# Kernel optimization log

Measured on AMD Instinct MI355X. Metric: run time of the kernel, lower is better.

Reference implementation:

```python
import jax, jax.numpy as jnp
import numpy as np

N_NODES = 50000
N_EDGES = 800000
IN_DIM = 256
HID = 128


def setup_inputs() -> dict:
    key = jax.random.key(0)
    ks = jax.random.split(key, 8)
    x = jax.random.normal(ks[0], (N_NODES, IN_DIM), dtype=jnp.float32)
    edge_index = jax.random.randint(ks[1], (2, N_EDGES), 0, N_NODES, dtype=jnp.int32)
    edge_weight = jax.random.uniform(ks[2], (N_EDGES,), dtype=jnp.float32)
    # xavier_normal with gain=1.414 as in torch init
    g = 1.414
    W1 = jax.random.normal(ks[3], (HID, IN_DIM), dtype=jnp.float32) * (g * np.sqrt(2.0 / (HID + IN_DIM)))
    W2 = jax.random.normal(ks[4], (HID, HID), dtype=jnp.float32) * (g * np.sqrt(2.0 / (HID + HID)))
    b1 = jnp.zeros((HID,), dtype=jnp.float32)
    b2 = jnp.zeros((HID,), dtype=jnp.float32)
    a1 = jnp.full((1,), 0.25, dtype=jnp.float32)  # nn.PReLU() default init
    a2 = jnp.full((1,), 0.25, dtype=jnp.float32)
    return {"x": x, "edge_index": edge_index, "edge_weight": edge_weight,
            "W1": W1, "b1": b1, "a1": a1, "W2": W2, "b2": b2, "a2": a2}


def _gcn_layer(z, W, b, a, src, dst, w):
    # linear (no bias): [N, out]
    fts = z @ W.T
    # spmm: out[dst] += w * fts[src]
    msg = fts[src] * w[:, None]                      # [E, out]
    out = jax.ops.segment_sum(msg, dst, num_segments=N_NODES) + b
    # PReLU (single shared parameter)
    return jnp.where(out >= 0, out, a * out)


def reference(x, edge_index, edge_weight, W1, b1, a1, W2, b2, a2):
    src, dst = edge_index[0], edge_index[1]
    z = _gcn_layer(x, W1, b1, a1, src, dst, edge_weight)
    z = _gcn_layer(z, W2, b2, a2, src, dst, edge_weight)
    return z
```

## Files before the change

### kernel.cpp

```cpp
#include <hip/hip_runtime.h>
#include <hip/hip_bf16.h>

#define HID 128
#define BSH 6
#define BSZ 64
#define NBMAX 1024
#define HB 64

typedef unsigned int uint;
typedef unsigned short ushort;
typedef __attribute__((ext_vector_type(8))) short short8;
typedef __attribute__((ext_vector_type(4))) float f32x4;

__device__ __forceinline__ ushort bf16_of(float x) {
    return __bfloat16_as_ushort(__float2bfloat16(x));
}

__device__ __forceinline__ uint pack_bf16x2(float a, float b) {
    return (uint)bf16_of(a) | ((uint)bf16_of(b) << 16);
}

union FragAB { uint4 u; short8 s; };

__global__ __launch_bounds__(256) void pack_hist(
    const float* __restrict__ W1, const float* __restrict__ W2,
    ushort* __restrict__ Wb1, ushort* __restrict__ Wb2,
    const int* __restrict__ dst, int* __restrict__ hpart, int E, int NB) {
    int blk = blockIdx.x;
    if (blk >= 24) {
        __shared__ int h[NBMAX];
        int hb = blk - 24;
        for (int i = threadIdx.x; i < NB; i += 256) h[i] = 0;
        __syncthreads();
        int chunk = (E + HB - 1) / HB;
        int c0 = hb * chunk;
        int c1 = min(c0 + chunk, E);
        for (int e = c0 + threadIdx.x; e < c1; e += 256)
            atomicAdd(&h[dst[e] >> BSH], 1);
        __syncthreads();
        for (int i = threadIdx.x; i < NB; i += 256) hpart[hb * NBMAX + i] = h[i];
        return;
    }
    const float* W = (blk < 16) ? W1 : W2;
    ushort* Wb = (blk < 16) ? Wb1 : Wb2;
    int K = (blk < 16) ? 256 : 128;
    int t = ((blk < 16) ? blk : blk - 16) * 256 + threadIdx.x;
    int lane = t & 63, f = t >> 6;
    int s = f >> 3, c = f & 7;
    int m = c * 16 + (lane & 15);
    int k0 = s * 32 + (lane >> 4) * 8;
    const float* wr = W + (size_t)m * K + k0;
    float4 a = *(const float4*)wr;
    float4 b = *(const float4*)(wr + 4);
    uint4 o = make_uint4(pack_bf16x2(a.x, a.y), pack_bf16x2(a.z, a.w),
                         pack_bf16x2(b.x, b.y), pack_bf16x2(b.z, b.w));
    *(uint4*)(Wb + (size_t)t * 8) = o;
}

template <int K, bool ABF16>
__device__ __forceinline__ FragAB load_afrag(const void* __restrict__ Xv, int row,
                                             int k0, bool ok) {
    FragAB af;
    if (ABF16) {
        af.u = ok ? *(const uint4*)((const ushort*)Xv + (size_t)row * K + k0)
                  : make_uint4(0, 0, 0, 0);
    } else {
        float4 va = make_float4(0.f, 0.f, 0.f, 0.f), vb = va;
        if (ok) {
            const float* xr = (const float*)Xv + (size_t)row * K + k0;
            va = *(const float4*)xr;
            vb = *(const float4*)(xr + 4);
        }
        af.u = make_uint4(pack_bf16x2(va.x, va.y), pack_bf16x2(va.z, va.w),
                          pack_bf16x2(vb.x, vb.y), pack_bf16x2(vb.z, vb.w));
    }
    return af;
}

template <int K, bool ABF16>
__global__ __launch_bounds__(256) void gemm_mfma(
    const void* __restrict__ Xv, const ushort* __restrict__ Wb,
    ushort* __restrict__ out, int N) {
    const int lane = threadIdx.x & 63;
    const int wid  = threadIdx.x >> 6;
    const int n0   = blockIdx.x * 128 + wid * 32;
    const int r0 = n0 + (lane & 15);
    const int r1 = r0 + 16;
    const bool ok0 = r0 < N, ok1 = r1 < N;
    const int kgrp = (lane >> 4) * 8;

    f32x4 acc0[8], acc1[8];
#pragma unroll
    for (int c = 0; c < 8; ++c) {
        acc0[c] = (f32x4){0.f, 0.f, 0.f, 0.f};
        acc1[c] = (f32x4){0.f, 0.f, 0.f, 0.f};
    }

#pragma unroll
    for (int s = 0; s < K / 32; ++s) {
        const int k0 = s * 32 + kgrp;
        FragAB a0 = load_afrag<K, ABF16>(Xv, r0, k0, ok0);
        FragAB a1 = load_afrag<K, ABF16>(Xv, r1, k0, ok1);
#pragma unroll
        for (int c = 0; c < 8; ++c) {
            FragAB bfr;
            bfr.u = *(const uint4*)(Wb + (size_t)((s * 8 + c) * 64 + lane) * 8);
            acc0[c] = __builtin_amdgcn_mfma_f32_16x16x32_bf16(a0.s, bfr.s, acc0[c], 0, 0, 0);
            acc1[c] = __builtin_amdgcn_mfma_f32_16x16x32_bf16(a1.s, bfr.s, acc1[c], 0, 0, 0);
        }
    }
    const int col = lane & 15;
    const int rb0 = n0 + (lane >> 4) * 4;
#pragma unroll
    for (int c = 0; c < 8; ++c) {
#pragma unroll
        for (int r = 0; r < 4; ++r) {
            int na = rb0 + r;
            if (na < N) out[(size_t)na * HID + c * 16 + col] = bf16_of(acc0[c][r]);
            int nb = na + 16;
            if (nb < N) out[(size_t)nb * HID + c * 16 + col] = bf16_of(acc1[c][r]);
        }
    }
}

__global__ __launch_bounds__(NBMAX) void bucket_scan(const int* __restrict__ hpart,
                                                     int* __restrict__ gbase,
                                                     int* __restrict__ gcur, int NB, int E) {
    __shared__ int l[NBMAX];
    int t = threadIdx.x;
    int v = 0;
    if (t < NB)
        for (int b = 0; b < HB; ++b) v += hpart[b * NBMAX + t];
    l[t] = v;
    __syncthreads();
    int x = v;
    for (int o = 1; o < NBMAX; o <<= 1) {
        int y = (t >= o) ? l[t - o] : 0;
        __syncthreads();
        x += y;
        l[t] = x;
        __syncthreads();
    }
    if (t < NB) { gbase[t] = x - v; gcur[t] = x - v; }
    if (t == 0) gbase[NB] = E;
}

__global__ __launch_bounds__(256) void bucket_stage(
    const int* __restrict__ src, const int* __restrict__ dst,
    const float* __restrict__ w, int* __restrict__ gcur,
    int2* __restrict__ staged, int E, int NB) {
    __shared__ int lh[NBMAX], lb[NBMAX];
    for (int i = threadIdx.x; i < NB; i += 256) lh[i] = 0;
    __syncthreads();
    int chunk = (E + gridDim.x - 1) / gridDim.x;
    int c0 = blockIdx.x * chunk;
    int c1 = min(c0 + chunk, E);
    for (int e = c0 + threadIdx.x; e < c1; e += 256)
        atomicAdd(&lh[dst[e] >> BSH], 1);
    __syncthreads();
    for (int i = threadIdx.x; i < NB; i += 256) {
        int c = lh[i];
        lb[i] = c ? atomicAdd(&gcur[i], c) : 0;
        lh[i] = 0;
    }
    __syncthreads();
    for (int e = c0 + threadIdx.x; e < c1; e += 256) {
        int d = dst[e];
        int b = d >> BSH;
        int slot = lb[b] + atomicAdd(&lh[b], 1);
        staged[slot] = make_int2(src[e] | ((d & (BSZ - 1)) << 16), __float_as_int(w[e]));
    }
}

__global__ __launch_bounds__(256) void node_sort(
    const int* __restrict__ gbase, const int2* __restrict__ staged,
    int2* __restrict__ csr, int* __restrict__ off, int N) {
    __shared__ int hist[BSZ];
    __shared__ int cur[BSZ];
    const int b = blockIdx.x;
    const int s0 = gbase[b], s1 = gbase[b + 1];
    const int t = threadIdx.x;
    if (t < BSZ) hist[t] = 0;
    __syncthreads();
    for (int e = s0 + t; e < s1; e += 256)
        atomicAdd(&hist[(staged[e].x >> 16) & (BSZ - 1)], 1);
    __syncthreads();
    if (t < BSZ) {
        int x = hist[t];
        int incl = x;
#pragma unroll
        for (int o = 1; o < BSZ; o <<= 1) {
            int y = __shfl_up(incl, o, BSZ);
            if (t >= o) incl += y;
        }
        int excl = incl - x;
        cur[t] = excl;
        int n = (b << BSH) + t;
        if (n <= N) off[n] = s0 + excl;
    }
    __syncthreads();
    for (int e = s0 + t; e < s1; e += 256) {
        int2 m = staged[e];
        int d = (m.x >> 16) & (BSZ - 1);
        int p = atomicAdd(&cur[d], 1);
        csr[s0 + p] = m;
    }
}

template <bool OUTBF16>
__global__ __launch_bounds__(256) void csr_gather_bf16(
    const int* __restrict__ off, const int2* __restrict__ edges,
    const ushort* __restrict__ fts, void* __restrict__ outv,
    const float* __restrict__ bias, const float* __restrict__ alpha, int N) {
    int d = blockIdx.x * 4 + (threadIdx.x >> 6);
    if (d >= N) return;
    const int lane = threadIdx.x & 63;
    const int g = lane >> 4;
    const int sub = lane & 15;
    int p = off[d];
    const int end = off[d + 1];
    float acc[8];
#pragma unroll
    for (int j = 0; j < 8; ++j) acc[j] = 0.f;

#define LOBITS(u_) __uint_as_float((u_) << 16)
#define HIBITS(u_) __uint_as_float((u_) & 0xffff0000u)
#define ROWOF(M_) (*(const uint4*)(fts + (size_t)((M_).x & 0xffff) * HID + sub * 8))
#define ACC8(R_, W_)                                              \
    do {                                                          \
        acc[0] += (W_) * LOBITS((R_).x); acc[1] += (W_) * HIBITS((R_).x); \
        acc[2] += (W_) * LOBITS((R_).y); acc[3] += (W_) * HIBITS((R_).y); \
        acc[4] += (W_) * LOBITS((R_).z); acc[5] += (W_) * HIBITS((R_).z); \
        acc[6] += (W_) * LOBITS((R_).w); acc[7] += (W_) * HIBITS((R_).w); \
    } while (0)

    for (; p + 16 <= end; p += 16) {
        int2 m0 = edges[p + g], m1 = edges[p + 4 + g];
        int2 m2 = edges[p + 8 + g], m3 = edges[p + 12 + g];
        uint4 r0 = ROWOF(m0), r1 = ROWOF(m1), r2 = ROWOF(m2), r3 = ROWOF(m3);
        float w0 = __int_as_float(m0.y), w1 = __int_as_float(m1.y);
        float w2 = __int_as_float(m2.y), w3 = __int_as_float(m3.y);
        ACC8(r0, w0); ACC8(r1, w1); ACC8(r2, w2); ACC8(r3, w3);
    }
    for (; p + 8 <= end; p += 8) {
        int2 ma = edges[p + g];
        int2 mb = edges[p + 4 + g];
        uint4 ra = ROWOF(ma), rb = ROWOF(mb);
        float wa = __int_as_float(ma.y), wb = __int_as_float(mb.y);
        ACC8(ra, wa);
        ACC8(rb, wb);
    }
    for (; p < end; p += 4) {
        int i = p + g;
        int2 m = edges[(i < end) ? i : (end - 1)];
        float wt = (i < end) ? __int_as_float(m.y) : 0.f;
        uint4 r = ROWOF(m);
        ACC8(r, wt);
    }
#undef ACC8
#undef ROWOF
#undef LOBITS
#undef HIBITS

#pragma unroll
    for (int j = 0; j < 8; ++j) {
        acc[j] += __shfl_xor(acc[j], 16);
        acc[j] += __shfl_xor(acc[j], 32);
    }

    const float a = alpha[0];
#pragma unroll
    for (int j = 0; j < 8; ++j) {
        float v = acc[j] + bias[sub * 8 + j];
        acc[j] = v >= 0.f ? v : a * v;
    }
    if (g == 0) {
        if (OUTBF16) {
            uint4 o = make_uint4(pack_bf16x2(acc[0], acc[1]), pack_bf16x2(acc[2], acc[3]),
                                 pack_bf16x2(acc[4], acc[5]), pack_bf16x2(acc[6], acc[7]));
            *(uint4*)((ushort*)outv + (size_t)d * HID + sub * 8) = o;
        } else {
            float* op = (float*)outv + (size_t)d * HID + sub * 8;
            *(float4*)op = make_float4(acc[0], acc[1], acc[2], acc[3]);
            *(float4*)(op + 4) = make_float4(acc[4], acc[5], acc[6], acc[7]);
        }
    }
}

extern "C" void kernel_launch(void* const* d_in, const int* in_sizes, int n_in,
                              void* d_out, int out_size, void* d_ws, size_t ws_size,
                              hipStream_t stream) {
    const float* x  = (const float*)d_in[0];
    const int*   ei = (const int*)d_in[1];
    const float* ew = (const float*)d_in[2];
    const float* W1 = (const float*)d_in[3];
    const float* b1 = (const float*)d_in[4];
    const float* a1 = (const float*)d_in[5];
    const float* W2 = (const float*)d_in[6];
    const float* b2 = (const float*)d_in[7];
    const float* a2 = (const float*)d_in[8];
    float* out = (float*)d_out;

    int N = in_sizes[0] / 256;
    int E = in_sizes[2];
    const int* src = ei;
    const int* dst = ei + E;
    int NB = (N + BSZ - 1) >> BSH;

    ushort* fts    = (ushort*)d_ws;
    ushort* agg    = fts + (size_t)N * HID;
    int2*   staged = (int2*)(agg + (size_t)N * HID);
    int2*   csr    = staged + E;
    ushort* Wb1    = (ushort*)(csr + E);
    ushort* Wb2    = Wb1 + 128 * 256;
    int*    hpart  = (int*)(Wb2 + 128 * 128);
    int*    gbase  = hpart + HB * NBMAX;
    int*    gcur   = gbase + NBMAX + 1;
    int*    off    = gcur + NBMAX;

    pack_hist<<<24 + HB, 256, 0, stream>>>(W1, W2, Wb1, Wb2, dst, hpart, E, NB);

    bucket_scan<<<1, NBMAX, 0, stream>>>(hpart, gbase, gcur, NB, E);
    bucket_stage<<<128, 256, 0, stream>>>(src, dst, ew, gcur, staged, E, NB);
    node_sort<<<NB, 256, 0, stream>>>(gbase, staged, csr, off, N);

    int gblk = (N + 127) / 128;
    int ggrid = (N + 3) / 4;

    gemm_mfma<256, false><<<gblk, 256, 0, stream>>>(x, Wb1, fts, N);
    csr_gather_bf16<true><<<ggrid, 256, 0, stream>>>(off, csr, fts, agg, b1, a1, N);

    gemm_mfma<128, true><<<gblk, 256, 0, stream>>>(agg, Wb2, fts, N);
    csr_gather_bf16<false><<<ggrid, 256, 0, stream>>>(off, csr, fts, out, b2, a2, N);
}
```

Before: 154.0 us.

## Fuse layer-1 GEMM with edge bucket staging into one heterogeneous launch

Merges the first-layer MFMA GEMM and the bucket_stage edge scatter into a single kernel whose blocks are split by block index, so the compute-bound GEMM and the atomic-heavy staging can run concurrently on the GPU. This removes one launch and the serialization between two independent stages. In exchange, the GEMM blocks now carry the staging kernel's 8KB static shared memory, which may reduce occupancy, and the GEMM blocks are scheduled before the staging blocks.

```diff
diff --git a/kernel.cpp b/kernel.cpp
--- a/kernel.cpp
+++ b/kernel.cpp
@@ -6,6 +6,7 @@
 #define BSZ 64
 #define NBMAX 1024
 #define HB 64
+#define STAGE_BLKS 128
 
 typedef unsigned int uint;
 typedef unsigned short ushort;
@@ -78,12 +79,12 @@
 }
 
 template <int K, bool ABF16>
-__global__ __launch_bounds__(256) void gemm_mfma(
+__device__ __forceinline__ void gemm_body(
     const void* __restrict__ Xv, const ushort* __restrict__ Wb,
-    ushort* __restrict__ out, int N) {
+    ushort* __restrict__ out, int N, int bid) {
     const int lane = threadIdx.x & 63;
     const int wid  = threadIdx.x >> 6;
-    const int n0   = blockIdx.x * 128 + wid * 32;
+    const int n0   = bid * 128 + wid * 32;
     const int r0 = n0 + (lane & 15);
     const int r1 = r0 + 16;
     const bool ok0 = r0 < N, ok1 = r1 < N;
@@ -121,6 +122,54 @@
             if (nb < N) out[(size_t)nb * HID + c * 16 + col] = bf16_of(acc1[c][r]);
         }
     }
+}
+
+__device__ __forceinline__ void stage_body(
+    const int* __restrict__ src, const int* __restrict__ dst,
+    const float* __restrict__ w, int* __restrict__ gcur,
+    int2* __restrict__ staged, int E, int NB, int bid) {
+    __shared__ int lh[NBMAX], lb[NBMAX];
+    for (int i = threadIdx.x; i < NB; i += 256) lh[i] = 0;
+    __syncthreads();
+    int chunk = (E + STAGE_BLKS - 1) / STAGE_BLKS;
+    int c0 = bid * chunk;
+    int c1 = min(c0 + chunk, E);
+    for (int e = c0 + threadIdx.x; e < c1; e += 256)
+        atomicAdd(&lh[dst[e] >> BSH], 1);
+    __syncthreads();
+    for (int i = threadIdx.x; i < NB; i += 256) {
+        int c = lh[i];
+        lb[i] = c ? atomicAdd(&gcur[i], c) : 0;
+        lh[i] = 0;
+    }
+    __syncthreads();
+    for (int e = c0 + threadIdx.x; e < c1; e += 256) {
+        int d = dst[e];
+        int b = d >> BSH;
+        int slot = lb[b] + atomicAdd(&lh[b], 1);
+        staged[slot] = make_int2(src[e] | ((d & (BSZ - 1)) << 16), __float_as_int(w[e]));
+    }
+}
+
+__global__ __launch_bounds__(256) void gemm1_stage(
+    const float* __restrict__ X, const ushort* __restrict__ Wb1,
+    ushort* __restrict__ fts, int N, int gblk,
+    const int* __restrict__ src, const int* __restrict__ dst,
+    const float* __restrict__ w, int* __restrict__ gcur,
+    int2* __restrict__ staged, int E, int NB) {
+    int bid = blockIdx.x;
+    if (bid < gblk) {
+        gemm_body<256, false>(X, Wb1, fts, N, bid);
+    } else {
+        stage_body(src, dst, w, gcur, staged, E, NB, bid - gblk);
+    }
+}
+
+template <int K, bool ABF16>
+__global__ __launch_bounds__(256) void gemm_mfma(
+    const void* __restrict__ Xv, const ushort* __restrict__ Wb,
+    ushort* __restrict__ out, int N) {
+    gemm_body<K, ABF16>(Xv, Wb, out, N, blockIdx.x);
 }
 
 __global__ __launch_bounds__(NBMAX) void bucket_scan(const int* __restrict__ hpart,
@@ -143,33 +192,6 @@
     }
     if (t < NB) { gbase[t] = x - v; gcur[t] = x - v; }
     if (t == 0) gbase[NB] = E;
-}
-
-__global__ __launch_bounds__(256) void bucket_stage(
-    const int* __restrict__ src, const int* __restrict__ dst,
-    const float* __restrict__ w, int* __restrict__ gcur,
-    int2* __restrict__ staged, int E, int NB) {
-    __shared__ int lh[NBMAX], lb[NBMAX];
-    for (int i = threadIdx.x; i < NB; i += 256) lh[i] = 0;
-    __syncthreads();
-    int chunk = (E + gridDim.x - 1) / gridDim.x;
-    int c0 = blockIdx.x * chunk;
-    int c1 = min(c0 + chunk, E);
-    for (int e = c0 + threadIdx.x; e < c1; e += 256)
-        atomicAdd(&lh[dst[e] >> BSH], 1);
-    __syncthreads();
-    for (int i = threadIdx.x; i < NB; i += 256) {
-        int c = lh[i];
-        lb[i] = c ? atomicAdd(&gcur[i], c) : 0;
-        lh[i] = 0;
-    }
-    __syncthreads();
-    for (int e = c0 + threadIdx.x; e < c1; e += 256) {
-        int d = dst[e];
-        int b = d >> BSH;
-        int slot = lb[b] + atomicAdd(&lh[b], 1);
-        staged[slot] = make_int2(src[e] | ((d & (BSZ - 1)) << 16), __float_as_int(w[e]));
-    }
 }
 
 __global__ __launch_bounds__(256) void node_sort(
@@ -318,18 +340,15 @@
     int*    gcur   = gbase + NBMAX + 1;
     int*    off    = gcur + NBMAX;
 
-    pack_hist<<<24 + HB, 256, 0, stream>>>(W1, W2, Wb1, Wb2, dst, hpart, E, NB);
-
-    bucket_scan<<<1, NBMAX, 0, stream>>>(hpart, gbase, gcur, NB, E);
-    bucket_stage<<<128, 256, 0, stream>>>(src, dst, ew, gcur, staged, E, NB);
-    node_sort<<<NB, 256, 0, stream>>>(gbase, staged, csr, off, N);
-
     int gblk = (N + 127) / 128;
     int ggrid = (N + 3) / 4;
 
-    gemm_mfma<256, false><<<gblk, 256, 0, stream>>>(x, Wb1, fts, N);
+    pack_hist<<<24 + HB, 256, 0, stream>>>(W1, W2, Wb1, Wb2, dst, hpart, E, NB);
+    bucket_scan<<<1, NBMAX, 0, stream>>>(hpart, gbase, gcur, NB, E);
+    gemm1_stage<<<gblk + STAGE_BLKS, 256, 0, stream>>>(
+        x, Wb1, fts, N, gblk, src, dst, ew, gcur, staged, E, NB);
+    node_sort<<<NB, 256, 0, stream>>>(gbase, staged, csr, off, N);
     csr_gather_bf16<true><<<ggrid, 256, 0, stream>>>(off, csr, fts, agg, b1, a1, N);
-
     gemm_mfma<128, true><<<gblk, 256, 0, stream>>>(agg, Wb2, fts, N);
     csr_gather_bf16<false><<<ggrid, 256, 0, stream>>>(off, csr, fts, out, b2, a2, N);
 }
```

Result: faster. 141.7 us (-8.0%).
